# Kernel tuning notes

Measured on AMD Instinct MI355X. Metric: run time of the kernel, lower is better.

The kernel has to match this reference:

```python
import jax, jax.numpy as jnp
import numpy as np

B, IN, H, CTX = 16384, 1024, 1024, 2048


def setup_inputs() -> dict:
    key = jax.random.key(0)
    ks = jax.random.split(key, 20)
    stdv = 1.0 / np.sqrt(H)
    u = lambda k, shape: jax.random.uniform(k, shape, jnp.float32, -stdv, stdv)
    inp = {
        "y": jax.random.normal(ks[0], (B, IN), jnp.float32),
        "ctx": jax.random.normal(ks[1], (B, CTX), jnp.float32),
        "c0": jax.random.normal(ks[2], (B, H), jnp.float32),
        "h0": jax.random.normal(ks[3], (B, H), jnp.float32),
        # Concatenated gate weights in order (i, f, o, c), matching the
        # per-gate matrices Wi..Wc, Ui..Uc, Ci..Cc of the original module.
        "W": u(ks[4], (4 * H, IN)),   # input projections
        "U": u(ks[5], (4 * H, H)),    # hidden projections
        "C": u(ks[6], (4 * H, CTX)),  # context projections
        "b": u(ks[7], (4 * H,)),      # gate biases
    }
    return inp


def reference(y, ctx, c0, h0, W, U, C, b):
    # One fused GEMM per input stream instead of 12 small ones; same math.
    gates = y @ W.T + h0 @ U.T + ctx @ C.T + b  # [B, 4H]
    gi, gf, go, gc = jnp.split(gates, 4, axis=-1)
    i = jax.nn.sigmoid(gi)
    f = jax.nn.sigmoid(gf)
    o = jax.nn.sigmoid(go)
    c_hat = jnp.tanh(gc)
    c = i * c_hat + f * c0
    h = o * jnp.tanh(c)
    return (c, h)
```

## Files before the change

kernel.cpp:

```cpp
#include <hip/hip_runtime.h>
#include <hip/hip_bf16.h>
#include <stdint.h>

typedef __attribute__((ext_vector_type(8))) short short8;
typedef __attribute__((ext_vector_type(8))) unsigned short ushort8;
typedef __attribute__((ext_vector_type(4))) float f32x4;
typedef __attribute__((ext_vector_type(8))) __bf16 bf16x8;

#define GAS __attribute__((address_space(1)))
#define LAS __attribute__((address_space(3)))

static constexpr int Bn = 16384;
static constexpr int Hn = 1024;
static constexpr int KT = 4096;
static constexpr int BM = 256;
static constexpr int BK = 64;
static constexpr int NT = KT / BK;

#define SBAR()   asm volatile("s_barrier" ::: "memory")
#define LGKM0()  asm volatile("s_waitcnt lgkmcnt(0)" ::: "memory")
#define VMCNT(n) asm volatile("s_waitcnt vmcnt(" #n ")" ::: "memory")

__device__ __forceinline__ unsigned short f2bf(float f) {
  unsigned u = __builtin_bit_cast(unsigned, f);
  u = (u + 0x7FFFu + ((u >> 16) & 1u)) >> 16;
  return (unsigned short)u;
}

__device__ __forceinline__ float sigm(float x) { return 1.f / (1.f + __expf(-x)); }

__global__ __launch_bounds__(256) void cvt_concat_k(
    const float* __restrict__ s0, const float* __restrict__ s1,
    const float* __restrict__ s2, unsigned short* __restrict__ dst,
    long long n8) {
  long long stride = (long long)gridDim.x * blockDim.x;
  for (long long g = (long long)blockIdx.x * blockDim.x + threadIdx.x; g < n8;
       g += stride) {
    long long row = g >> 9;
    int cg = (int)(g & 511) << 3;
    const float* src;
    if (cg < 1024)      src = s0 + row * 1024 + cg;
    else if (cg < 2048) src = s1 + row * 1024 + (cg - 1024);
    else                src = s2 + row * 2048 + (cg - 2048);
    float4 f0 = *(const float4*)src;
    float4 f1 = *(const float4*)(src + 4);
    ushort8 o;
    o[0] = f2bf(f0.x); o[1] = f2bf(f0.y); o[2] = f2bf(f0.z); o[3] = f2bf(f0.w);
    o[4] = f2bf(f1.x); o[5] = f2bf(f1.y); o[6] = f2bf(f1.z); o[7] = f2bf(f1.w);
    *(ushort8*)(dst + (g << 3)) = o;
  }
}

__global__ __launch_bounds__(512, 2) void lstm_gemm(
    const unsigned short* __restrict__ X, const unsigned short* __restrict__ Wc,
    const float* __restrict__ bias, const float* __restrict__ c0,
    float* __restrict__ out_c, float* __restrict__ out_h) {
  extern __shared__ char smem[];

  int bid = blockIdx.x;
  int swz = (bid & 7) * 128 + (bid >> 3);
  int mblk = swz >> 4, cblk = swz & 15;
  int brow0 = mblk * BM;
  int hcol0 = cblk * 64;

  int tid = threadIdx.x;
  int lane = tid & 63, wid = tid >> 6;
  int wr = wid >> 2, wc = wid & 3;

  const char* Xc = (const char*)X;
  const char* Wcc = (const char*)Wc;

  int rr = tid >> 3;
  uint32_t cbyte = (uint32_t)(((tid & 7) * 16) ^ ((rr & 7) << 4));
  uint32_t aoff[2][2], boff[2][2];
#pragma unroll
  for (int half = 0; half < 2; ++half) {
#pragma unroll
    for (int j = 0; j < 2; ++j) {
      int r = half * 128 + j * 64 + rr;
      aoff[half][j] = (uint32_t)(brow0 + r) * (KT * 2) + cbyte;
      int w = ((r >> 4) & 3) * 1024 + hcol0 + ((r >> 6) << 4) + (r & 15);
      boff[half][j] = (uint32_t)w * (KT * 2) + cbyte;
    }
  }

  auto stage_half = [&](int isB, int half, int kt, int bufs) {
#pragma unroll
    for (int j = 0; j < 2; ++j) {
      uint32_t off = (isB ? boff[half][j] : aoff[half][j]) + (uint32_t)kt * 128u;
      const char* src = (isB ? Wcc : Xc) + off;
      char* dst = smem + bufs * 65536 + isB * 32768 + half * 16384 + j * 8192 +
                  wid * 1024;
      __builtin_amdgcn_global_load_lds((const GAS unsigned int*)src,
                                       (LAS unsigned int*)dst, 16, 0, 0);
    }
  };

  int kg = (lane >> 4) << 4;
  int sw = (lane & 7) << 4;
  int koff0 = (0 + kg) ^ sw;
  int koff1 = (64 + kg) ^ sw;
  int fr = lane & 15;

  f32x4 acc[8][4] = {};
  short8 bfr[4][2];

  stage_half(1, 0, 0, 0);
  stage_half(1, 1, 0, 0);
  stage_half(0, 0, 0, 0);
  stage_half(0, 1, 0, 0);
  VMCNT(2);
  SBAR();

  for (int t = 0; t < NT; ++t) {
    int p = t & 1;
    bool last = (t == NT - 1);
#pragma unroll
    for (int q = 0; q < 4; ++q) {
      if (q == 0) {
        int bb = p * 65536 + 32768 + (wc * 64 + fr) * 128;
#pragma unroll
        for (int n = 0; n < 4; ++n) {
          bfr[n][0] = *(const short8*)(smem + bb + n * 2048 + koff0);
          bfr[n][1] = *(const short8*)(smem + bb + n * 2048 + koff1);
        }
      }
      int ab = p * 65536 + ((2 * q + wr) * 32 + fr) * 128;
      short8 a0k0 = *(const short8*)(smem + ab + koff0);
      short8 a0k1 = *(const short8*)(smem + ab + koff1);
      short8 a1k0 = *(const short8*)(smem + ab + 2048 + koff0);
      short8 a1k1 = *(const short8*)(smem + ab + 2048 + koff1);

      if (!last) stage_half(q < 2 ? 1 : 0, q & 1, t + 1, p ^ 1);

      SBAR();
      LGKM0();
      __builtin_amdgcn_s_setprio(1);
#pragma unroll
      for (int n = 0; n < 4; ++n) {
        acc[2 * q][n] = __builtin_amdgcn_mfma_f32_16x16x32_bf16(
            __builtin_bit_cast(bf16x8, a0k0), __builtin_bit_cast(bf16x8, bfr[n][0]),
            acc[2 * q][n], 0, 0, 0);
        acc[2 * q][n] = __builtin_amdgcn_mfma_f32_16x16x32_bf16(
            __builtin_bit_cast(bf16x8, a0k1), __builtin_bit_cast(bf16x8, bfr[n][1]),
            acc[2 * q][n], 0, 0, 0);
        acc[2 * q + 1][n] = __builtin_amdgcn_mfma_f32_16x16x32_bf16(
            __builtin_bit_cast(bf16x8, a1k0), __builtin_bit_cast(bf16x8, bfr[n][0]),
            acc[2 * q + 1][n], 0, 0, 0);
        acc[2 * q + 1][n] = __builtin_amdgcn_mfma_f32_16x16x32_bf16(
            __builtin_bit_cast(bf16x8, a1k1), __builtin_bit_cast(bf16x8, bfr[n][1]),
            acc[2 * q + 1][n], 0, 0, 0);
      }
      __builtin_amdgcn_s_setprio(0);

      if (q == 1) {
        if (last) { VMCNT(0); } else { VMCNT(4); }
      } else if (q == 3 && !last) {
        VMCNT(2);
      }
      SBAR();
    }
  }

  int col = hcol0 + wc * 16 + fr;
  float bi = bias[col], bf_ = bias[1024 + col];
  float bo = bias[2048 + col], bc = bias[3072 + col];
#pragma unroll
  for (int m = 0; m < 8; ++m) {
    int row0 = brow0 + (2 * (m >> 1) + wr) * 32 + (m & 1) * 16 + ((lane >> 4) << 2);
#pragma unroll
    for (int j = 0; j < 4; ++j) {
      size_t idx = (size_t)(row0 + j) * 1024 + col;
      float i_ = sigm(acc[m][0][j] + bi);
      float f_ = sigm(acc[m][1][j] + bf_);
      float o_ = sigm(acc[m][2][j] + bo);
      float ch = tanhf(acc[m][3][j] + bc);
      float cn = i_ * ch + f_ * c0[idx];
      out_c[idx] = cn;
      out_h[idx] = o_ * tanhf(cn);
    }
  }
}

__global__ __launch_bounds__(256) void lstm_naive(
    const float* __restrict__ y, const float* __restrict__ ctx,
    const float* __restrict__ c0, const float* __restrict__ h0,
    const float* __restrict__ W, const float* __restrict__ U,
    const float* __restrict__ C, const float* __restrict__ b,
    float* __restrict__ out_c, float* __restrict__ out_h) {
  size_t t = (size_t)blockIdx.x * blockDim.x + threadIdx.x;
  if (t >= (size_t)Bn * Hn) return;
  int row = (int)(t >> 10), col = (int)(t & 1023);
  float g[4];
#pragma unroll
  for (int gg = 0; gg < 4; ++gg) {
    int wrow = gg * 1024 + col;
    float s = b[wrow];
    const float* yr = y + (size_t)row * 1024;
    const float* Wr = W + (size_t)wrow * 1024;
    for (int k = 0; k < 1024; ++k) s += yr[k] * Wr[k];
    const float* hr = h0 + (size_t)row * 1024;
    const float* Ur = U + (size_t)wrow * 1024;
    for (int k = 0; k < 1024; ++k) s += hr[k] * Ur[k];
    const float* cr = ctx + (size_t)row * 2048;
    const float* Cr = C + (size_t)wrow * 2048;
    for (int k = 0; k < 2048; ++k) s += cr[k] * Cr[k];
    g[gg] = s;
  }
  float i_ = sigm(g[0]), f_ = sigm(g[1]), o_ = sigm(g[2]), ch = tanhf(g[3]);
  float cn = i_ * ch + f_ * c0[t];
  out_c[t] = cn;
  out_h[t] = o_ * tanhf(cn);
}

extern "C" void kernel_launch(void* const* d_in, const int* in_sizes, int n_in,
                              void* d_out, int out_size, void* d_ws, size_t ws_size,
                              hipStream_t stream) {
  const float* y   = (const float*)d_in[0];
  const float* ctx = (const float*)d_in[1];
  const float* c0  = (const float*)d_in[2];
  const float* h0  = (const float*)d_in[3];
  const float* W   = (const float*)d_in[4];
  const float* U   = (const float*)d_in[5];
  const float* C   = (const float*)d_in[6];
  const float* b   = (const float*)d_in[7];
  float* out = (float*)d_out;
  float* out_c = out;
  float* out_h = out + (size_t)Bn * Hn;

  const size_t needX = (size_t)Bn * KT * 2;
  const size_t needW = (size_t)(4 * Hn) * KT * 2;

  if (ws_size >= needX + needW) {
    unsigned short* Xb = (unsigned short*)d_ws;
    unsigned short* Wb = (unsigned short*)((char*)d_ws + needX);
    cvt_concat_k<<<2048, 256, 0, stream>>>(y, h0, ctx, Xb, (long long)Bn * 512);
    cvt_concat_k<<<2048, 256, 0, stream>>>(W, U, C, Wb, (long long)(4 * Hn) * 512);
    (void)hipFuncSetAttribute((const void*)lstm_gemm,
                              hipFuncAttributeMaxDynamicSharedMemorySize, 131072);
    lstm_gemm<<<1024, 512, 131072, stream>>>(Xb, Wb, b, c0, out_c, out_h);
  } else {
    lstm_naive<<<(Bn * Hn + 255) / 256, 256, 0, stream>>>(y, ctx, c0, h0, W, U, C,
                                                          b, out_c, out_h);
  }
}
```

Baseline: 629.8 us.

## Deepen global-to-LDS prefetch pipeline and use fast sigmoid/tanh epilogue

Stages the GEMM loads further ahead: prefetch now runs up to two K-tiles in advance with clamped tile indices, so the last-iteration branches go away and vmcnt waits are looser. It drops the explicit lgkmcnt(0) wait and replaces the inline-asm barrier with the builtin. The epilogue switches to rcp-based sigmoid and an exp-based tanh. The intent is to hide more global latency behind the MFMAs. The risks are LDS buffer hazards, since only two buffers exist while loads run two tiles ahead, reading LDS fragments without an explicit wait, and redundant tail loads.

```diff
diff --git a/kernel.cpp b/kernel.cpp
--- a/kernel.cpp
+++ b/kernel.cpp
@@ -14,11 +14,9 @@
 static constexpr int Hn = 1024;
 static constexpr int KT = 4096;
 static constexpr int BM = 256;
-static constexpr int BK = 64;
-static constexpr int NT = KT / BK;
-
-#define SBAR()   asm volatile("s_barrier" ::: "memory")
-#define LGKM0()  asm volatile("s_waitcnt lgkmcnt(0)" ::: "memory")
+static constexpr int NT = KT / 64;
+
+#define SBAR()   __builtin_amdgcn_s_barrier()
 #define VMCNT(n) asm volatile("s_waitcnt vmcnt(" #n ")" ::: "memory")
 
 __device__ __forceinline__ unsigned short f2bf(float f) {
@@ -27,7 +25,12 @@
   return (unsigned short)u;
 }
 
-__device__ __forceinline__ float sigm(float x) { return 1.f / (1.f + __expf(-x)); }
+__device__ __forceinline__ float fast_sigm(float x) {
+  return __builtin_amdgcn_rcpf(1.f + __expf(-x));
+}
+__device__ __forceinline__ float fast_tanh(float x) {
+  return 1.f - 2.f * __builtin_amdgcn_rcpf(__expf(2.f * x) + 1.f);
+}
 
 __global__ __launch_bounds__(256) void cvt_concat_k(
     const float* __restrict__ s0, const float* __restrict__ s1,
@@ -84,10 +87,12 @@
     }
   }
 
-  auto stage_half = [&](int isB, int half, int kt, int bufs) {
+  auto stage_half = [&](int isB, int half, int tt) {
+    int ts = tt < NT ? tt : NT - 1;
+    int bufs = tt & 1;
 #pragma unroll
     for (int j = 0; j < 2; ++j) {
-      uint32_t off = (isB ? boff[half][j] : aoff[half][j]) + (uint32_t)kt * 128u;
+      uint32_t off = (isB ? boff[half][j] : aoff[half][j]) + (uint32_t)ts * 128u;
       const char* src = (isB ? Wcc : Xc) + off;
       char* dst = smem + bufs * 65536 + isB * 32768 + half * 16384 + j * 8192 +
                   wid * 1024;
@@ -105,16 +110,18 @@
   f32x4 acc[8][4] = {};
   short8 bfr[4][2];
 
-  stage_half(1, 0, 0, 0);
-  stage_half(1, 1, 0, 0);
-  stage_half(0, 0, 0, 0);
-  stage_half(0, 1, 0, 0);
-  VMCNT(2);
+  stage_half(1, 0, 0);
+  stage_half(1, 1, 0);
+  stage_half(0, 0, 0);
+  stage_half(0, 1, 0);
+  stage_half(1, 0, 1);
+  stage_half(1, 1, 1);
+  stage_half(0, 0, 1);
+  VMCNT(8);
   SBAR();
 
   for (int t = 0; t < NT; ++t) {
     int p = t & 1;
-    bool last = (t == NT - 1);
 #pragma unroll
     for (int q = 0; q < 4; ++q) {
       if (q == 0) {
@@ -131,10 +138,12 @@
       short8 a1k0 = *(const short8*)(smem + ab + 2048 + koff0);
       short8 a1k1 = *(const short8*)(smem + ab + 2048 + koff1);
 
-      if (!last) stage_half(q < 2 ? 1 : 0, q & 1, t + 1, p ^ 1);
+      if (q == 0)      stage_half(0, 1, t + 1);
+      else if (q == 1) stage_half(1, 0, t + 2);
+      else if (q == 2) stage_half(1, 1, t + 2);
+      else             stage_half(0, 0, t + 2);
 
       SBAR();
-      LGKM0();
       __builtin_amdgcn_s_setprio(1);
 #pragma unroll
       for (int n = 0; n < 4; ++n) {
@@ -153,11 +162,8 @@
       }
       __builtin_amdgcn_s_setprio(0);
 
-      if (q == 1) {
-        if (last) { VMCNT(0); } else { VMCNT(4); }
-      } else if (q == 3 && !last) {
-        VMCNT(2);
-      }
+      if (q == 1) { VMCNT(10); }
+      else if (q == 3) { VMCNT(8); }
       SBAR();
     }
   }
@@ -171,13 +177,13 @@
 #pragma unroll
     for (int j = 0; j < 4; ++j) {
       size_t idx = (size_t)(row0 + j) * 1024 + col;
-      float i_ = sigm(acc[m][0][j] + bi);
-      float f_ = sigm(acc[m][1][j] + bf_);
-      float o_ = sigm(acc[m][2][j] + bo);
-      float ch = tanhf(acc[m][3][j] + bc);
+      float i_ = fast_sigm(acc[m][0][j] + bi);
+      float f_ = fast_sigm(acc[m][1][j] + bf_);
+      float o_ = fast_sigm(acc[m][2][j] + bo);
+      float ch = fast_tanh(acc[m][3][j] + bc);
       float cn = i_ * ch + f_ * c0[idx];
       out_c[idx] = cn;
-      out_h[idx] = o_ * tanhf(cn);
+      out_h[idx] = o_ * fast_tanh(cn);
     }
   }
 }
@@ -207,10 +213,11 @@
     for (int k = 0; k < 2048; ++k) s += cr[k] * Cr[k];
     g[gg] = s;
   }
-  float i_ = sigm(g[0]), f_ = sigm(g[1]), o_ = sigm(g[2]), ch = tanhf(g[3]);
+  float i_ = fast_sigm(g[0]), f_ = fast_sigm(g[1]);
+  float o_ = fast_sigm(g[2]), ch = fast_tanh(g[3]);
   float cn = i_ * ch + f_ * c0[t];
   out_c[t] = cn;
-  out_h[t] = o_ * tanhf(cn);
+  out_h[t] = o_ * fast_tanh(cn);
 }
 
 extern "C" void kernel_launch(void* const* d_in, const int* in_sizes, int n_in,
```

Result: faster. 557.2 us (-11.5%).
